# Performance work log

Hardware: AMD Instinct MI355X
Metric: run time of the kernel (lower is better)

Reference implementation:

```python
import jax, jax.numpy as jnp
import numpy as np
import math

B_, S_, I_, CS, CZ, H, D = 1, 128, 256, 256, 128, 8, 32
TOT = H * D
EPS = 1e-5

def _ln(x, g, b):
    mu = jnp.mean(x, axis=-1, keepdims=True)
    var = jnp.var(x, axis=-1, keepdims=True)
    return (x - mu) * jax.lax.rsqrt(var + EPS) * g + b

def setup_inputs() -> dict:
    key = jax.random.key(0)
    ks = jax.random.split(key, 10)
    sc = 0.02
    return {
        "msa": jax.random.normal(ks[0], (B_, S_, I_, CS), jnp.float32),
        "pair": jax.random.normal(ks[1], (B_, I_, I_, CZ), jnp.float32),
        "ln_m_g": jnp.ones((CS,), jnp.float32),
        "ln_m_b": jnp.zeros((CS,), jnp.float32),
        "ln_p_g": jnp.ones((CZ,), jnp.float32),
        "ln_p_b": jnp.zeros((CZ,), jnp.float32),
        "Wq": jax.random.normal(ks[2], (CS, TOT), jnp.float32) * sc,
        "Wk": jax.random.normal(ks[3], (CS, TOT), jnp.float32) * sc,
        "Wv": jax.random.normal(ks[4], (CS, TOT), jnp.float32) * sc,
        "Wp": jax.random.normal(ks[5], (CZ, H), jnp.float32) * sc,
        "Wg": jax.random.normal(ks[6], (CS, TOT), jnp.float32) * sc,
        "bg": jnp.zeros((TOT,), jnp.float32),
        "Wo": jax.random.normal(ks[7], (TOT, CS), jnp.float32) * sc,
        "bo": jnp.zeros((CS,), jnp.float32),
    }

def reference(msa, pair, ln_m_g, ln_m_b, ln_p_g, ln_p_b, Wq, Wk, Wv, Wp, Wg, bg, Wo, bo):
    b, s, i, _ = msa.shape
    m = _ln(msa, ln_m_g, ln_m_b)                                 # [b,s,i,cs]
    Q = (m @ Wq).reshape(b, s, i, H, D)
    K = (m @ Wk).reshape(b, s, i, H, D)
    V = (m @ Wv).reshape(b, s, i, H, D)
    G = jax.nn.sigmoid((m @ Wg + bg).reshape(b, s, i, H, D))
    p = _ln(pair, ln_p_g, ln_p_b)                                # [b,i,j,cz]
    bias = jnp.transpose(p @ Wp, (0, 3, 1, 2))[:, None]          # [b,1,h,i,j]
    scores = jnp.einsum('bsihd,bsjhd->bshij', Q, K) / math.sqrt(D) + bias
    attn = jax.nn.softmax(scores, axis=-1)                       # [b,s,h,i,j]
    vals = jnp.einsum('bshij,bsjhd->bsihd', attn, V)
    vals = (G * vals).reshape(b, s, i, TOT)
    return vals @ Wo + bo                                        # [b,s,i,cs]
```

## Files before the change

kernel.cpp:

```cpp
#include <hip/hip_runtime.h>


typedef _Float16 fp16;
typedef fp16 fp16x8 __attribute__((ext_vector_type(8)));
typedef fp16 fp16x4 __attribute__((ext_vector_type(4)));
typedef float floatx4 __attribute__((ext_vector_type(4)));

#define NM 8388608u

__device__ __forceinline__ void gld16(const fp16* g, fp16* l) {
  __builtin_amdgcn_global_load_lds(
      (const __attribute__((address_space(1))) unsigned int*)g,
      (__attribute__((address_space(3))) unsigned int*)l, 16, 0, 0);
}

__global__ __launch_bounds__(256) void ln_msa_k(const float* __restrict__ x,
    const float* __restrict__ g, const float* __restrict__ b,
    fp16* __restrict__ Am)
{
  int row  = blockIdx.x * 4 + (threadIdx.x >> 6);
  int lane = threadIdx.x & 63;
  int base = row * 256 + lane * 4;
  float4 v = *(const float4*)(x + base);
  float s  = (v.x + v.y) + (v.z + v.w);
  float ss = (v.x*v.x + v.y*v.y) + (v.z*v.z + v.w*v.w);
  #pragma unroll
  for (int mk = 32; mk >= 1; mk >>= 1) {
    s  += __shfl_xor(s, mk);
    ss += __shfl_xor(ss, mk);
  }
  float mu  = s * (1.0f/256.0f);
  float var = ss * (1.0f/256.0f) - mu*mu;
  float rs  = rsqrtf(var + 1e-5f);
  float4 gg = *(const float4*)(g + lane*4);
  float4 bb = *(const float4*)(b + lane*4);
  fp16x4 o;
  o[0] = (fp16)((v.x - mu) * rs * gg.x + bb.x);
  o[1] = (fp16)((v.y - mu) * rs * gg.y + bb.y);
  o[2] = (fp16)((v.z - mu) * rs * gg.z + bb.z);
  o[3] = (fp16)((v.w - mu) * rs * gg.w + bb.w);
  *(fp16x4*)(Am + (size_t)row * 256 + lane * 4) = o;
}

__global__ __launch_bounds__(256) void wprep_qkvg_k(const float* __restrict__ Wq,
    const float* __restrict__ Wk, const float* __restrict__ Wv,
    const float* __restrict__ Wg, fp16* __restrict__ WT)
{
  int n = blockIdx.x, k = threadIdx.x;
  const float* W = (n < 256) ? Wq : (n < 512) ? Wk : (n < 768) ? Wv : Wg;
  WT[(size_t)n * 256 + k] = (fp16)W[k * 256 + (n & 255)];
}

__global__ __launch_bounds__(256) void wprep_o_k(const float* __restrict__ Wo,
    fp16* __restrict__ WT)
{
  int n = blockIdx.x, k = threadIdx.x;
  WT[(size_t)n * 256 + k] = (fp16)Wo[k * 256 + n];
}

__global__ __launch_bounds__(256) void ln_pair_bias_k(const float* __restrict__ pair,
    const float* __restrict__ g, const float* __restrict__ b,
    const float* __restrict__ Wp, float* __restrict__ biasF)
{
  const int t = threadIdx.x;
  const int w = t >> 6, lane = t & 63;
  const int grp = lane >> 3, sub = lane & 7;
  const int row = blockIdx.x * 32 + w * 8 + grp;
  const int c0  = sub * 16;

  const float* pr = pair + (size_t)row * 128 + c0;
  float4 v[4];
  #pragma unroll
  for (int e = 0; e < 4; ++e) v[e] = *(const float4*)(pr + e*4);

  float s = 0.f, ss = 0.f;
  #pragma unroll
  for (int e = 0; e < 4; ++e) {
    s  += (v[e].x + v[e].y) + (v[e].z + v[e].w);
    ss += (v[e].x*v[e].x + v[e].y*v[e].y) + (v[e].z*v[e].z + v[e].w*v[e].w);
  }
  #pragma unroll
  for (int mk = 1; mk <= 4; mk <<= 1) {
    s  += __shfl_xor(s, mk);
    ss += __shfl_xor(ss, mk);
  }
  float mu  = s * (1.0f/128.0f);
  float var = ss * (1.0f/128.0f) - mu*mu;
  float rs  = rsqrtf(var + 1e-5f);

  float acc[8] = {0.f,0.f,0.f,0.f,0.f,0.f,0.f,0.f};
  #pragma unroll
  for (int e = 0; e < 4; ++e) {
    float4 gg = *(const float4*)(g + c0 + e*4);
    float4 bb = *(const float4*)(b + c0 + e*4);
    float p[4];
    p[0] = (v[e].x - mu) * rs * gg.x + bb.x;
    p[1] = (v[e].y - mu) * rs * gg.y + bb.y;
    p[2] = (v[e].z - mu) * rs * gg.z + bb.z;
    p[3] = (v[e].w - mu) * rs * gg.w + bb.w;
    #pragma unroll
    for (int u = 0; u < 4; ++u) {
      const float* wr = Wp + (c0 + e*4 + u) * 8;
      float4 w0 = *(const float4*)(wr);
      float4 w1 = *(const float4*)(wr + 4);
      acc[0] = fmaf(p[u], w0.x, acc[0]);
      acc[1] = fmaf(p[u], w0.y, acc[1]);
      acc[2] = fmaf(p[u], w0.z, acc[2]);
      acc[3] = fmaf(p[u], w0.w, acc[3]);
      acc[4] = fmaf(p[u], w1.x, acc[4]);
      acc[5] = fmaf(p[u], w1.y, acc[5]);
      acc[6] = fmaf(p[u], w1.z, acc[6]);
      acc[7] = fmaf(p[u], w1.w, acc[7]);
    }
  }
  #pragma unroll
  for (int mk = 1; mk <= 4; mk <<= 1)
    #pragma unroll
    for (int hh = 0; hh < 8; ++hh)
      acc[hh] += __shfl_xor(acc[hh], mk);

  int i = row >> 8, j = row & 255;
  biasF[sub * 65536 + (j >> 2) * 1024 + i * 4 + (j & 3)] = acc[sub];
}

__global__ __launch_bounds__(256, 3) void mfma_gemm_k(
    const fp16* __restrict__ A, const fp16* __restrict__ BT,
    fp16* __restrict__ qkv, fp16* __restrict__ gG, float* __restrict__ outF,
    const float* __restrict__ bvec, int mode)
{
  __shared__ fp16 As[128 * 32];
  __shared__ fp16 Bs[128 * 32];
  const int t  = threadIdx.x;
  const int bm = blockIdx.x * 128;
  const int bn = blockIdx.y * 128;
  const int lane = t & 63;
  const int w  = t >> 6;
  const int wm = (w & 1) * 64, wn = (w >> 1) * 64;
  const int r16 = lane & 15, q = lane >> 4;
  const int qa8 = (q ^ ((r16 >> 1) & 3)) * 8;

  floatx4 acc[4][4];
  #pragma unroll
  for (int i = 0; i < 4; ++i)
    #pragma unroll
    for (int j = 0; j < 4; ++j)
      acc[i][j] = (floatx4){0.f, 0.f, 0.f, 0.f};

  for (int kb = 0; kb < 256; kb += 32) {
    #pragma unroll
    for (int i2 = 0; i2 < 2; ++i2) {
      int c = i2 * 256 + t;
      int rr = c >> 2, qs = c & 3;
      int kq = (qs ^ ((rr >> 1) & 3)) << 3;
      gld16(A  + (size_t)(bm + rr) * 256 + kb + kq, As + c * 8);
      gld16(BT + (size_t)(bn + rr) * 256 + kb + kq, Bs + c * 8);
    }
    __syncthreads();
    fp16x8 af[4], bf[4];
    #pragma unroll
    for (int ti = 0; ti < 4; ++ti)
      af[ti] = *(const fp16x8*)&As[(wm + ti*16 + r16) * 32 + qa8];
    #pragma unroll
    for (int tj = 0; tj < 4; ++tj)
      bf[tj] = *(const fp16x8*)&Bs[(wn + tj*16 + r16) * 32 + qa8];
    #pragma unroll
    for (int ti = 0; ti < 4; ++ti)
      #pragma unroll
      for (int tj = 0; tj < 4; ++tj)
        acc[ti][tj] = __builtin_amdgcn_mfma_f32_16x16x32_f16(
            bf[tj], af[ti], acc[ti][tj], 0, 0, 0);
    __syncthreads();
  }

  if (mode == 0) {
    #pragma unroll
    for (int ti = 0; ti < 4; ++ti) {
      int m = bm + wm + ti*16 + r16;
      #pragma unroll
      for (int tj = 0; tj < 4; ++tj) {
        int n0 = bn + wn + tj*16 + q*4;
        int seg = n0 >> 8, c2 = n0 & 255;
        if (seg < 3) {
          fp16x4 pk;
          #pragma unroll
          for (int r = 0; r < 4; ++r) pk[r] = (fp16)acc[ti][tj][r];
          *(fp16x4*)(qkv + (size_t)seg * NM + (size_t)m * 256 + c2) = pk;
        } else {
          float4 bg4 = *(const float4*)(bvec + c2);
          fp16x4 o;
          o[0] = (fp16)(1.0f / (1.0f + __expf(-(acc[ti][tj][0] + bg4.x))));
          o[1] = (fp16)(1.0f / (1.0f + __expf(-(acc[ti][tj][1] + bg4.y))));
          o[2] = (fp16)(1.0f / (1.0f + __expf(-(acc[ti][tj][2] + bg4.z))));
          o[3] = (fp16)(1.0f / (1.0f + __expf(-(acc[ti][tj][3] + bg4.w))));
          *(fp16x4*)(gG + (size_t)(c2 >> 2) * 131072 + (size_t)m * 4) = o;
        }
      }
    }
  } else {
    #pragma unroll
    for (int ti = 0; ti < 4; ++ti) {
      int m = bm + wm + ti*16 + r16;
      #pragma unroll
      for (int tj = 0; tj < 4; ++tj) {
        int n0 = bn + wn + tj*16 + q*4;
        float4 bo4 = *(const float4*)(bvec + n0);
        float4 o;
        o.x = acc[ti][tj][0] + bo4.x;
        o.y = acc[ti][tj][1] + bo4.y;
        o.z = acc[ti][tj][2] + bo4.z;
        o.w = acc[ti][tj][3] + bo4.w;
        *(float4*)(outF + (size_t)m * 256 + n0) = o;
      }
    }
  }
}

__global__ __launch_bounds__(256, 4) void attn_k(
    const fp16* __restrict__ Q, const fp16* __restrict__ K,
    const fp16* __restrict__ V, const fp16* __restrict__ Gf,
    const float* __restrict__ biasF, fp16* __restrict__ gv)
{
  __shared__ fp16 Vt[32 * 256];
  __shared__ fp16 Pb[4][64 * 32];

  const int s = blockIdx.x, h = blockIdx.y;
  const int t = threadIdx.x;
  const int w = t >> 6, lane = t & 63;
  const int r16 = lane & 15, q = lane >> 4;
  const size_t base = ((size_t)s * 256) * 256 + h * 32;

  #pragma unroll
  for (int e = 0; e < 4; ++e) {
    int idx = e * 256 + t;
    int j = idx >> 2, d8 = (idx & 3) << 3;
    fp16x8 v = *(const fp16x8*)(V + base + (size_t)j * 256 + d8);
    #pragma unroll
    for (int u = 0; u < 8; ++u) {
      int d = d8 + u;
      Vt[d * 256 + (j ^ ((d & 7) << 3))] = v[u];
    }
  }
  __syncthreads();

  const int ibase = w * 64;
  fp16x8 qf[4];
  #pragma unroll
  for (int it = 0; it < 4; ++it)
    qf[it] = *(const fp16x8*)(Q + base + (size_t)(ibase + it*16 + r16) * 256 + q*8);

  floatx4 accO[2][4];
  #pragma unroll
  for (int dt = 0; dt < 2; ++dt)
    #pragma unroll
    for (int it = 0; it < 4; ++it)
      accO[dt][it] = (floatx4){0.f, 0.f, 0.f, 0.f};
  float lp[4] = {0.f, 0.f, 0.f, 0.f};

  fp16* pb = &Pb[w][0];
  const float scale = 0.17677669529663687f;
  const float* bp = biasF + h * 65536;

  for (int jc = 0; jc < 8; ++jc) {
    const int j0 = jc * 32;
    fp16x8 kf[2];
    #pragma unroll
    for (int jt = 0; jt < 2; ++jt)
      kf[jt] = *(const fp16x8*)(K + base + (size_t)(j0 + jt*16 + r16) * 256 + q*8);

    floatx4 sc[2][4];
    #pragma unroll
    for (int jt = 0; jt < 2; ++jt)
      #pragma unroll
      for (int it = 0; it < 4; ++it)
        sc[jt][it] = (floatx4){0.f, 0.f, 0.f, 0.f};
    #pragma unroll
    for (int jt = 0; jt < 2; ++jt)
      #pragma unroll
      for (int it = 0; it < 4; ++it)
        sc[jt][it] = __builtin_amdgcn_mfma_f32_16x16x32_f16(
            kf[jt], qf[it], sc[jt][it], 0, 0, 0);

    #pragma unroll
    for (int jt = 0; jt < 2; ++jt) {
      #pragma unroll
      for (int it = 0; it < 4; ++it) {
        int i  = ibase + it*16 + r16;
        int jb = j0 + jt*16 + q*4;
        int il = it*16 + r16;
        float4 b4 = *(const float4*)(bp + (jb >> 2) * 1024 + i * 4);
        float x0 = __expf(fmaf(sc[jt][it][0], scale, b4.x));
        float x1 = __expf(fmaf(sc[jt][it][1], scale, b4.y));
        float x2 = __expf(fmaf(sc[jt][it][2], scale, b4.z));
        float x3 = __expf(fmaf(sc[jt][it][3], scale, b4.w));
        lp[it] += (x0 + x1) + (x2 + x3);
        fp16x4 p4;
        p4[0] = (fp16)x0; p4[1] = (fp16)x1; p4[2] = (fp16)x2; p4[3] = (fp16)x3;
        int colw = (jt*16 + q*4) ^ (((il >> 1) & 3) << 3);
        *(fp16x4*)&pb[il * 32 + colw] = p4;
      }
    }

    fp16x8 vf[2], pf[4];
    #pragma unroll
    for (int dt = 0; dt < 2; ++dt) {
      int d = dt*16 + r16;
      vf[dt] = *(const fp16x8*)&Vt[d * 256 + ((j0 + q*8) ^ ((d & 7) << 3))];
    }
    #pragma unroll
    for (int it = 0; it < 4; ++it) {
      int il = it*16 + r16;
      pf[it] = *(const fp16x8*)&pb[il * 32 + ((q*8) ^ (((il >> 1) & 3) << 3))];
    }
    #pragma unroll
    for (int dt = 0; dt < 2; ++dt)
      #pragma unroll
      for (int it = 0; it < 4; ++it)
        accO[dt][it] = __builtin_amdgcn_mfma_f32_16x16x32_f16(
            vf[dt], pf[it], accO[dt][it], 0, 0, 0);
  }

  #pragma unroll
  for (int mk = 16; mk <= 32; mk <<= 1)
    #pragma unroll
    for (int it = 0; it < 4; ++it)
      lp[it] += __shfl_xor(lp[it], mk);

  #pragma unroll
  for (int it = 0; it < 4; ++it) {
    float invl = 1.0f / lp[it];
    int i = ibase + it*16 + r16;
    size_t row = (size_t)s * 256 + i;
    #pragma unroll
    for (int dt = 0; dt < 2; ++dt) {
      int d0 = h*32 + dt*16 + q*4;
      fp16x4 g4 = *(const fp16x4*)(Gf + (size_t)(d0 >> 2) * 131072 + row * 4);
      fp16x4 o4;
      #pragma unroll
      for (int r = 0; r < 4; ++r)
        o4[r] = (fp16)((float)g4[r] * accO[dt][it][r] * invl);
      *(fp16x4*)(gv + row * 256 + d0) = o4;
    }
  }
}

extern "C" void kernel_launch(void* const* d_in, const int* in_sizes, int n_in,
                              void* d_out, int out_size, void* d_ws, size_t ws_size,
                              hipStream_t stream) {
  const float* msa    = (const float*)d_in[0];
  const float* pair   = (const float*)d_in[1];
  const float* ln_m_g = (const float*)d_in[2];
  const float* ln_m_b = (const float*)d_in[3];
  const float* ln_p_g = (const float*)d_in[4];
  const float* ln_p_b = (const float*)d_in[5];
  const float* Wq     = (const float*)d_in[6];
  const float* Wk     = (const float*)d_in[7];
  const float* Wv     = (const float*)d_in[8];
  const float* Wp     = (const float*)d_in[9];
  const float* Wg     = (const float*)d_in[10];
  const float* bg     = (const float*)d_in[11];
  const float* Wo     = (const float*)d_in[12];
  const float* bo     = (const float*)d_in[13];
  float* out = (float*)d_out;

  char* wsb = (char*)d_ws;
  fp16*  Am      = (fp16*)(wsb);
  fp16*  QKV16   = (fp16*)(wsb + 16777216);
  fp16*  Gfb     = (fp16*)(wsb + 67108864);
  float* biasF   = (float*)(wsb + 83886080);
  fp16*  WqkvgT  = (fp16*)(wsb + 85983232);
  fp16*  WoT     = (fp16*)(wsb + 86507520);
  fp16*  gvp     = Am;

  ln_msa_k<<<8192, 256, 0, stream>>>(msa, ln_m_g, ln_m_b, Am);
  wprep_qkvg_k<<<1024, 256, 0, stream>>>(Wq, Wk, Wv, Wg, WqkvgT);
  wprep_o_k<<<256, 256, 0, stream>>>(Wo, WoT);
  ln_pair_bias_k<<<2048, 256, 0, stream>>>(pair, ln_p_g, ln_p_b, Wp, biasF);

  mfma_gemm_k<<<dim3(256, 8), 256, 0, stream>>>(Am, WqkvgT, QKV16, Gfb,
                                                nullptr, bg, 0);

  attn_k<<<dim3(128, 8), 256, 0, stream>>>(QKV16, QKV16 + NM, QKV16 + 2*NM,
                                           Gfb, biasF, gvp);

  mfma_gemm_k<<<dim3(256, 2), 256, 0, stream>>>(gvp, WoT, nullptr, nullptr,
                                                out, bo, 1);
}
```

Before: 239.7 us.

## Triple-buffer LDS tiles in MFMA GEMM with async prefetch two stages ahead

Replaces the single-buffered load/compute loop in the projection GEMM with a three-buffer pipeline. Global-to-LDS loads run two K-tiles ahead, with explicit vmcnt waits and one barrier per iteration instead of two, and global addresses are precomputed once. The goal is to hide global load latency behind MFMA work and cut synchronization. LDS use triples to 48KB per block, which may reduce occupancy relative to the launch bound of 3 blocks.

```diff
diff --git a/kernel.cpp b/kernel.cpp
--- a/kernel.cpp
+++ b/kernel.cpp
@@ -128,8 +128,8 @@
     fp16* __restrict__ qkv, fp16* __restrict__ gG, float* __restrict__ outF,
     const float* __restrict__ bvec, int mode)
 {
-  __shared__ fp16 As[128 * 32];
-  __shared__ fp16 Bs[128 * 32];
+  __shared__ fp16 As[3][128 * 32];
+  __shared__ fp16 Bs[3][128 * 32];
   const int t  = threadIdx.x;
   const int bm = blockIdx.x * 128;
   const int bn = blockIdx.y * 128;
@@ -139,6 +139,15 @@
   const int r16 = lane & 15, q = lane >> 4;
   const int qa8 = (q ^ ((r16 >> 1) & 3)) * 8;
 
+  const int ca = t,        ra = ca >> 2;
+  const int cb = 256 + t,  rb = cb >> 2;
+  const int ka = ((ca & 3) ^ ((ra >> 1) & 3)) << 3;
+  const int kc = ((cb & 3) ^ ((rb >> 1) & 3)) << 3;
+  const fp16* gA0 = A  + (size_t)(bm + ra) * 256 + ka;
+  const fp16* gA1 = A  + (size_t)(bm + rb) * 256 + kc;
+  const fp16* gB0 = BT + (size_t)(bn + ra) * 256 + ka;
+  const fp16* gB1 = BT + (size_t)(bn + rb) * 256 + kc;
+
   floatx4 acc[4][4];
   #pragma unroll
   for (int i = 0; i < 4; ++i)
@@ -146,31 +155,40 @@
     for (int j = 0; j < 4; ++j)
       acc[i][j] = (floatx4){0.f, 0.f, 0.f, 0.f};
 
-  for (int kb = 0; kb < 256; kb += 32) {
-    #pragma unroll
-    for (int i2 = 0; i2 < 2; ++i2) {
-      int c = i2 * 256 + t;
-      int rr = c >> 2, qs = c & 3;
-      int kq = (qs ^ ((rr >> 1) & 3)) << 3;
-      gld16(A  + (size_t)(bm + rr) * 256 + kb + kq, As + c * 8);
-      gld16(BT + (size_t)(bn + rr) * 256 + kb + kq, Bs + c * 8);
-    }
-    __syncthreads();
+  #define STAGE(buf, kb) do {                      \
+    gld16(gA0 + (kb), &As[buf][ca * 8]);           \
+    gld16(gB0 + (kb), &Bs[buf][ca * 8]);           \
+    gld16(gA1 + (kb), &As[buf][cb * 8]);           \
+    gld16(gB1 + (kb), &Bs[buf][cb * 8]); } while (0)
+
+  STAGE(0, 0);
+  STAGE(1, 32);
+
+  #pragma unroll
+  for (int kt = 0; kt < 8; ++kt) {
+    if (kt < 7) asm volatile("s_waitcnt vmcnt(4)" ::: "memory");
+    else        asm volatile("s_waitcnt vmcnt(0)" ::: "memory");
+    __builtin_amdgcn_s_barrier();
+    __builtin_amdgcn_sched_barrier(0);
+    if (kt < 6) {
+      STAGE((kt + 2) % 3, (kt + 2) * 32);
+    }
+    const int cbuf = kt % 3;
     fp16x8 af[4], bf[4];
     #pragma unroll
     for (int ti = 0; ti < 4; ++ti)
-      af[ti] = *(const fp16x8*)&As[(wm + ti*16 + r16) * 32 + qa8];
+      af[ti] = *(const fp16x8*)&As[cbuf][(wm + ti*16 + r16) * 32 + qa8];
     #pragma unroll
     for (int tj = 0; tj < 4; ++tj)
-      bf[tj] = *(const fp16x8*)&Bs[(wn + tj*16 + r16) * 32 + qa8];
+      bf[tj] = *(const fp16x8*)&Bs[cbuf][(wn + tj*16 + r16) * 32 + qa8];
     #pragma unroll
     for (int ti = 0; ti < 4; ++ti)
       #pragma unroll
       for (int tj = 0; tj < 4; ++tj)
         acc[ti][tj] = __builtin_amdgcn_mfma_f32_16x16x32_f16(
             bf[tj], af[ti], acc[ti][tj], 0, 0, 0);
-    __syncthreads();
-  }
+  }
+  #undef STAGE
 
   if (mode == 0) {
     #pragma unroll
```

Result: no change. 238.4 us (-0.6%).

## Widen GEMM K-step to 64, template N-tile, merge weight-prep kernels

Applied to the files above, without the earlier changes.

The GEMM now loads two 32-wide K slices per barrier pair, which halves the number of __syncthreads per tile, and precomputes the global load addresses outside the loop. It is templated on the N tile width so the output projection uses a 64-wide N tile, doubling its grid to 1024 blocks for better CU occupancy. The two weight-transpose kernels are merged into a single launch to save launch overhead. The cost is doubled LDS per block, which may reduce occupancy, and less B-operand reuse for the narrower tile.

```diff
diff --git a/kernel.cpp b/kernel.cpp
--- a/kernel.cpp
+++ b/kernel.cpp
@@ -42,20 +42,19 @@
   *(fp16x4*)(Am + (size_t)row * 256 + lane * 4) = o;
 }
 
-__global__ __launch_bounds__(256) void wprep_qkvg_k(const float* __restrict__ Wq,
+__global__ __launch_bounds__(256) void wprep_k(const float* __restrict__ Wq,
     const float* __restrict__ Wk, const float* __restrict__ Wv,
-    const float* __restrict__ Wg, fp16* __restrict__ WT)
+    const float* __restrict__ Wg, const float* __restrict__ Wo,
+    fp16* __restrict__ WT, fp16* __restrict__ WoT)
 {
   int n = blockIdx.x, k = threadIdx.x;
-  const float* W = (n < 256) ? Wq : (n < 512) ? Wk : (n < 768) ? Wv : Wg;
-  WT[(size_t)n * 256 + k] = (fp16)W[k * 256 + (n & 255)];
-}
-
-__global__ __launch_bounds__(256) void wprep_o_k(const float* __restrict__ Wo,
-    fp16* __restrict__ WT)
-{
-  int n = blockIdx.x, k = threadIdx.x;
-  WT[(size_t)n * 256 + k] = (fp16)Wo[k * 256 + n];
+  if (n < 1024) {
+    const float* W = (n < 256) ? Wq : (n < 512) ? Wk : (n < 768) ? Wv : Wg;
+    WT[(size_t)n * 256 + k] = (fp16)W[k * 256 + (n & 255)];
+  } else {
+    int n2 = n - 1024;
+    WoT[(size_t)n2 * 256 + k] = (fp16)Wo[k * 256 + n2];
+  }
 }
 
 __global__ __launch_bounds__(256) void ln_pair_bias_k(const float* __restrict__ pair,
@@ -123,52 +122,64 @@
   biasF[sub * 65536 + (j >> 2) * 1024 + i * 4 + (j & 3)] = acc[sub];
 }
 
+template<int TJ>
 __global__ __launch_bounds__(256, 3) void mfma_gemm_k(
     const fp16* __restrict__ A, const fp16* __restrict__ BT,
     fp16* __restrict__ qkv, fp16* __restrict__ gG, float* __restrict__ outF,
     const float* __restrict__ bvec, int mode)
 {
-  __shared__ fp16 As[128 * 32];
-  __shared__ fp16 Bs[128 * 32];
+  __shared__ fp16 As[2][128 * 32];
+  __shared__ fp16 Bs[2][TJ * 32 * 32];
   const int t  = threadIdx.x;
   const int bm = blockIdx.x * 128;
-  const int bn = blockIdx.y * 128;
+  const int bn = blockIdx.y * (32 * TJ);
   const int lane = t & 63;
   const int w  = t >> 6;
-  const int wm = (w & 1) * 64, wn = (w >> 1) * 64;
+  const int wm = (w & 1) * 64, wn = (w >> 1) * (16 * TJ);
   const int r16 = lane & 15, q = lane >> 4;
   const int qa8 = (q ^ ((r16 >> 1) & 3)) * 8;
 
-  floatx4 acc[4][4];
+  const int ca = t,        ra = ca >> 2;
+  const int cb = 256 + t,  rb = cb >> 2;
+  const int ka = ((ca & 3) ^ ((ra >> 1) & 3)) << 3;
+  const int kc = ((cb & 3) ^ ((rb >> 1) & 3)) << 3;
+  const fp16* gA0 = A  + (size_t)(bm + ra) * 256 + ka;
+  const fp16* gA1 = A  + (size_t)(bm + rb) * 256 + kc;
+  const fp16* gB0 = BT + (size_t)(bn + ra) * 256 + ka;
+  const fp16* gB1 = BT + (size_t)(bn + rb) * 256 + kc;
+
+  floatx4 acc[4][TJ];
   #pragma unroll
   for (int i = 0; i < 4; ++i)
     #pragma unroll
-    for (int j = 0; j < 4; ++j)
+    for (int j = 0; j < TJ; ++j)
       acc[i][j] = (floatx4){0.f, 0.f, 0.f, 0.f};
 
-  for (int kb = 0; kb < 256; kb += 32) {
-    #pragma unroll
-    for (int i2 = 0; i2 < 2; ++i2) {
-      int c = i2 * 256 + t;
-      int rr = c >> 2, qs = c & 3;
-      int kq = (qs ^ ((rr >> 1) & 3)) << 3;
-      gld16(A  + (size_t)(bm + rr) * 256 + kb + kq, As + c * 8);
-      gld16(BT + (size_t)(bn + rr) * 256 + kb + kq, Bs + c * 8);
+  for (int kb = 0; kb < 256; kb += 64) {
+    #pragma unroll
+    for (int h = 0; h < 2; ++h) {
+      gld16(gA0 + kb + h*32, &As[h][ca * 8]);
+      gld16(gA1 + kb + h*32, &As[h][cb * 8]);
+      gld16(gB0 + kb + h*32, &Bs[h][ca * 8]);
+      if (TJ == 4) gld16(gB1 + kb + h*32, &Bs[h][cb * 8]);
     }
     __syncthreads();
-    fp16x8 af[4], bf[4];
-    #pragma unroll
-    for (int ti = 0; ti < 4; ++ti)
-      af[ti] = *(const fp16x8*)&As[(wm + ti*16 + r16) * 32 + qa8];
-    #pragma unroll
-    for (int tj = 0; tj < 4; ++tj)
-      bf[tj] = *(const fp16x8*)&Bs[(wn + tj*16 + r16) * 32 + qa8];
-    #pragma unroll
-    for (int ti = 0; ti < 4; ++ti)
-      #pragma unroll
-      for (int tj = 0; tj < 4; ++tj)
-        acc[ti][tj] = __builtin_amdgcn_mfma_f32_16x16x32_f16(
-            bf[tj], af[ti], acc[ti][tj], 0, 0, 0);
+    #pragma unroll
+    for (int h = 0; h < 2; ++h) {
+      fp16x8 af[4], bf[TJ];
+      #pragma unroll
+      for (int ti = 0; ti < 4; ++ti)
+        af[ti] = *(const fp16x8*)&As[h][(wm + ti*16 + r16) * 32 + qa8];
+      #pragma unroll
+      for (int tj = 0; tj < TJ; ++tj)
+        bf[tj] = *(const fp16x8*)&Bs[h][(wn + tj*16 + r16) * 32 + qa8];
+      #pragma unroll
+      for (int ti = 0; ti < 4; ++ti)
+        #pragma unroll
+        for (int tj = 0; tj < TJ; ++tj)
+          acc[ti][tj] = __builtin_amdgcn_mfma_f32_16x16x32_f16(
+              bf[tj], af[ti], acc[ti][tj], 0, 0, 0);
+    }
     __syncthreads();
   }
 
@@ -177,7 +188,7 @@
     for (int ti = 0; ti < 4; ++ti) {
       int m = bm + wm + ti*16 + r16;
       #pragma unroll
-      for (int tj = 0; tj < 4; ++tj) {
+      for (int tj = 0; tj < TJ; ++tj) {
         int n0 = bn + wn + tj*16 + q*4;
         int seg = n0 >> 8, c2 = n0 & 255;
         if (seg < 3) {
@@ -201,7 +212,7 @@
     for (int ti = 0; ti < 4; ++ti) {
       int m = bm + wm + ti*16 + r16;
       #pragma unroll
-      for (int tj = 0; tj < 4; ++tj) {
+      for (int tj = 0; tj < TJ; ++tj) {
         int n0 = bn + wn + tj*16 + q*4;
         float4 bo4 = *(const float4*)(bvec + n0);
         float4 o;
@@ -372,16 +383,15 @@
   fp16*  gvp     = Am;
 
   ln_msa_k<<<8192, 256, 0, stream>>>(msa, ln_m_g, ln_m_b, Am);
-  wprep_qkvg_k<<<1024, 256, 0, stream>>>(Wq, Wk, Wv, Wg, WqkvgT);
-  wprep_o_k<<<256, 256, 0, stream>>>(Wo, WoT);
+  wprep_k<<<1280, 256, 0, stream>>>(Wq, Wk, Wv, Wg, Wo, WqkvgT, WoT);
   ln_pair_bias_k<<<2048, 256, 0, stream>>>(pair, ln_p_g, ln_p_b, Wp, biasF);
 
-  mfma_gemm_k<<<dim3(256, 8), 256, 0, stream>>>(Am, WqkvgT, QKV16, Gfb,
-                                                nullptr, bg, 0);
+  mfma_gemm_k<4><<<dim3(256, 8), 256, 0, stream>>>(Am, WqkvgT, QKV16, Gfb,
+                                                   nullptr, bg, 0);
 
   attn_k<<<dim3(128, 8), 256, 0, stream>>>(QKV16, QKV16 + NM, QKV16 + 2*NM,
                                            Gfb, biasF, gvp);
 
-  mfma_gemm_k<<<dim3(256, 2), 256, 0, stream>>>(gvp, WoT, nullptr, nullptr,
-                                                out, bo, 1);
-}
+  mfma_gemm_k<2><<<dim3(256, 4), 256, 0, stream>>>(gvp, WoT, nullptr, nullptr,
+                                                   out, bo, 1);
+}
```

After: 234.9 us. 2.0% less time.
